# Kernel optimization log

Measured on AMD Instinct MI355X. Metric: run time of the kernel, lower is better.

The kernel has to match this reference:

```python
import jax, jax.numpy as jnp
import numpy as np

H, B, S, E, V, C = 1024, 1024, 128, 6, 3, 10


def setup_inputs() -> dict:
    key = jax.random.key(0)
    ks = jax.random.split(key, 18)
    sH = 1.0 / np.sqrt(H)

    def n(k, shape, scale):
        return (jax.random.normal(k, shape, dtype=jnp.float32) * scale)

    return {
        'x': jax.random.randint(ks[0], (B, S), 0, V),
        'emb': n(ks[1], (V, E), 1.0),
        'W_gx': n(ks[2], (H, E), 1.0 / np.sqrt(E)),
        'W_gh': n(ks[3], (H, H), sH),
        'b_g': n(ks[4], (H, 1), sH),
        'W_ix': n(ks[5], (H, E), 1.0 / np.sqrt(E)),
        'W_ih': n(ks[6], (H, H), sH),
        'b_i': n(ks[7], (H, 1), sH),
        'W_fx': n(ks[8], (H, E), 1.0 / np.sqrt(E)),
        'W_fh': n(ks[9], (H, H), sH),
        'b_f': n(ks[10], (H, 1), sH),
        'W_ox': n(ks[11], (H, E), 1.0 / np.sqrt(E)),
        'W_oh': n(ks[12], (H, H), sH),
        'b_o': n(ks[13], (H, 1), sH),
        'W_ph': n(ks[14], (C, H), sH),
        'b_p': n(ks[15], (C, 1), sH),
        'h_init': n(ks[16], (H, B), 1.0),
        'c_init': n(ks[17], (H, B), 1.0),
    }


def reference(x, emb, W_gx, W_gh, b_g, W_ix, W_ih, b_i, W_fx, W_fh, b_f,
              W_ox, W_oh, b_o, W_ph, b_p, h_init, c_init):
    T = x.shape[1] - 1  # torch loop runs over seq_length - 1 steps
    e = emb[x[:, :T]]  # [B, T, E]
    # Precompute all input-to-gate projections in one batched contraction each.
    Xg = jnp.einsum('he,bte->thb', W_gx, e)  # [T, H, B]
    Xi = jnp.einsum('he,bte->thb', W_ix, e)
    Xf = jnp.einsum('he,bte->thb', W_fx, e)
    Xo = jnp.einsum('he,bte->thb', W_ox, e)

    def step(carry, xs):
        h, c = carry  # [H, B]
        xg, xi, xf, xo = xs
        g = jnp.tanh(xg + W_gh @ h + b_g)
        i = jax.nn.sigmoid(xi + W_ih @ h + b_i)
        f = jax.nn.sigmoid(xf + W_fh @ h + b_f)
        o = jax.nn.sigmoid(xo + W_oh @ h + b_o)
        c2 = g * i + c * f
        h2 = jnp.tanh(c2) * o
        return (h2, c2), None

    (h, c), _ = jax.lax.scan(step, (h_init, c_init), (Xg, Xi, Xf, Xo))
    p = W_ph @ h + b_p  # [C, B]
    return jax.nn.log_softmax(p.T, axis=-1)  # [B, C]
```

## Files before the change

kernel.cpp:

```cpp
#include <hip/hip_runtime.h>

constexpr int kH = 1024;
constexpr int kB = 1024;
constexpr int kS = 128;
constexpr int kT = 127;
constexpr int kE = 6;
constexpr int kV = 3;
constexpr int kC = 10;

typedef short s16x8 __attribute__((ext_vector_type(8)));
typedef short s16x4 __attribute__((ext_vector_type(4)));
typedef float f32x4 __attribute__((ext_vector_type(4)));
typedef int   i32x2 __attribute__((ext_vector_type(2)));
typedef unsigned short u16;

__device__ __forceinline__ float b2f(u16 u) {
    return __uint_as_float(((unsigned)u) << 16);
}
__device__ __forceinline__ u16 f2b(float f) {
    unsigned u = __float_as_uint(f);
    return (u16)((u + 0x7FFFu + ((u >> 16) & 1u)) >> 16);
}
__device__ __forceinline__ float sigmoid_fast(float x) {
    return 1.0f / (1.0f + __expf(-x));
}
__device__ __forceinline__ float tanh_fast(float x) {
    return 2.0f / (1.0f + __expf(-2.0f * x)) - 1.0f;
}
__device__ __forceinline__ float clamp30(float x) {
    return fminf(fmaxf(x, -30.0f), 30.0f);
}

__device__ __forceinline__ void async_copy16(const u16* g, u16* l) {
    __builtin_amdgcn_global_load_lds(
        (const __attribute__((address_space(1))) void*)g,
        (__attribute__((address_space(3))) void*)l, 16, 0, 0);
}

__global__ __launch_bounds__(256) void prep_weights(
    const float* __restrict__ Wgh, const float* __restrict__ Wih,
    const float* __restrict__ Wfh, const float* __restrict__ Woh,
    u16* __restrict__ wsw)
{
    unsigned grp = blockIdx.x * 256 + threadIdx.x;
    const int lane = grp & 63;
    const int lm   = lane & 15;
    const int quad = lane >> 4;
    const int k0   = (grp >> 6) & 7;
    const int g    = (grp >> 9) & 3;
    const int kc   = (grp >> 11) & 3;
    const int by   = grp >> 13;
    const float* src = (g == 0) ? Wgh : (g == 1) ? Wih : (g == 2) ? Wfh : Woh;
    const int row = by * 16 + lm;
    const int k   = kc * 256 + k0 * 32 + quad * 8;
    f32x4 v0 = *(const f32x4*)(src + (size_t)row * kH + k);
    f32x4 v1 = *(const f32x4*)(src + (size_t)row * kH + k + 4);
    s16x8 o;
#pragma unroll
    for (int j = 0; j < 4; ++j) o[j] = (short)f2b(v0[j]);
#pragma unroll
    for (int j = 0; j < 4; ++j) o[4 + j] = (short)f2b(v1[j]);
    *(s16x8*)(wsw + (size_t)grp * 8) = o;
}

__global__ __launch_bounds__(1024) void prep_hc(
    const float* __restrict__ h0, const float* __restrict__ c0,
    u16* __restrict__ hA, float* __restrict__ cT)
{
    __shared__ float th[32][33];
    __shared__ float tc[32][33];
    int b = blockIdx.x * 32 + threadIdx.x;
    int h = blockIdx.y * 32 + threadIdx.y;
    th[threadIdx.y][threadIdx.x] = h0[(size_t)h * kB + b];
    tc[threadIdx.y][threadIdx.x] = c0[(size_t)h * kB + b];
    __syncthreads();
    int ob = blockIdx.x * 32 + threadIdx.y;
    int oh = blockIdx.y * 32 + threadIdx.x;
    hA[(size_t)ob * kH + oh] = f2b(th[threadIdx.x][threadIdx.y]);
    cT[(size_t)ob * kH + oh] = tc[threadIdx.x][threadIdx.y];
}

__global__ __launch_bounds__(256) void prep_q(
    const float* __restrict__ Wgx, const float* __restrict__ Wix,
    const float* __restrict__ Wfx, const float* __restrict__ Wox,
    const float* __restrict__ bg,  const float* __restrict__ bi,
    const float* __restrict__ bf_, const float* __restrict__ bo,
    const float* __restrict__ emb, float* __restrict__ Qp,
    int* __restrict__ ctrl)
{
    int tid = blockIdx.x * blockDim.x + threadIdx.x;
    if (tid < 512) ctrl[tid] = 0;
    if (tid >= 4096) return;
    int g   = tid >> 10;
    int hr4 = (tid & 1023) >> 2;
    int v   = tid & 3;
    const float* Wx = (g == 0) ? Wgx : (g == 1) ? Wix : (g == 2) ? Wfx : Wox;
    const float* bb = (g == 0) ? bg  : (g == 1) ? bi  : (g == 2) ? bf_ : bo;
    f32x4 o;
#pragma unroll
    for (int reg = 0; reg < 4; ++reg) {
        int row = hr4 * 4 + reg;
        float s = bb[row];
        if (v < kV) {
#pragma unroll
            for (int e = 0; e < kE; ++e) s += Wx[row * kE + e] * emb[v * kE + e];
        }
        o[reg] = s;
    }
    *(f32x4*)(Qp + (size_t)tid * 4) = o;
}

__global__ __launch_bounds__(512, 2) void lstm_persist(
    const u16* __restrict__ wsw, const float* __restrict__ Qp,
    const int* __restrict__ x,
    short* __restrict__ hA, short* __restrict__ hB,
    const float* __restrict__ cT, int* __restrict__ ctrl)
{
    __shared__ u16 wlds[65536];
    __shared__ int sh_ids[2];

    const int tid  = threadIdx.x;
    const int lane = tid & 63;
    const int wave = tid >> 6;
    const int lm   = lane & 15;
    const int quad = lane >> 4;

    if (tid == 0) {
        unsigned xccr;
        asm volatile("s_getreg_b32 %0, hwreg(HW_REG_XCC_ID)" : "=s"(xccr));
        int rank = atomicAdd(ctrl + 264 + (xccr & 7), 1);
        sh_ids[0] = (int)(xccr & 7);
        sh_ids[1] = rank;
    }
    __syncthreads();
    const int xcc  = sh_ids[0];
    const int rank = sh_ids[1];
    const int p    = xcc >> 1;
    const int q    = (xcc & 1) * 32 + rank;
    const bool leader = (rank == 0);
    const int r0 = q * 16;
    const int c0 = p * 256 + wave * 32;

    int* flags   = ctrl;
    int* release = ctrl + 256;

    const u16* wswblk = wsw + (size_t)q * 65536;

#pragma unroll
    for (int rr = 0; rr < 16; ++rr) {
        const int ub = wave * 8192 + rr * 512;
        async_copy16(wswblk + ub + lane * 8, &wlds[ub]);
    }

    f32x4 creg[2];
#pragma unroll
    for (int nt = 0; nt < 2; ++nt)
        creg[nt] = *(const f32x4*)(cT +
            (size_t)(c0 + nt * 16 + lm) * kH + r0 + quad * 4);

    const int* xp0 = x + (size_t)(c0 + lm) * kS;
    const int* xp1 = x + (size_t)(c0 + 16 + lm) * kS;
    const int koff = quad * 8;

    asm volatile("s_waitcnt vmcnt(0)" ::: "memory");
    __syncthreads();

#pragma unroll 1
    for (int t = 0; t < kT; ++t) {
        const short* hin  = (t & 1) ? hB : hA;
        short*       hout = (t & 1) ? hA : hB;

        const short* hrow0 = hin + (size_t)(c0 + lm) * kH + koff;
        const short* hrow1 = hin + (size_t)(c0 + 16 + lm) * kH + koff;
        s16x8 br[12][2];
#pragma unroll
        for (int s = 0; s < 10; ++s) {
            br[s][0] = *(const s16x8*)(hrow0 + s * 32);
            br[s][1] = *(const s16x8*)(hrow1 + s * 32);
        }

        int vv[2];
        {
            int v0 = xp0[t]; vv[0] = (v0 < 0) ? 0 : (v0 > kV - 1) ? (kV - 1) : v0;
            int v1 = xp1[t]; vv[1] = (v1 < 0) ? 0 : (v1 > kV - 1) ? (kV - 1) : v1;
        }
        f32x4 qv[2][4];
#pragma unroll
        for (int nt = 0; nt < 2; ++nt)
#pragma unroll
            for (int g = 0; g < 4; ++g)
                qv[nt][g] = *(const f32x4*)(Qp +
                    (size_t)(((g * 256 + q * 4 + quad) * 4 + vv[nt]) * 4));

        f32x4 acc[4][2];
        const f32x4 zero = {0.f, 0.f, 0.f, 0.f};
#pragma unroll
        for (int g = 0; g < 4; ++g)
#pragma unroll
            for (int n = 0; n < 2; ++n) acc[g][n] = zero;

#pragma unroll
        for (int k0 = 0; k0 < 32; ++k0) {
            if (k0 + 10 < 32) {
                const int s = (k0 + 10) % 12;
                br[s][0] = *(const s16x8*)(hrow0 + (k0 + 10) * 32);
                br[s][1] = *(const s16x8*)(hrow1 + (k0 + 10) * 32);
            }
            const int cur = k0 % 12;
            const int cb = (k0 >> 3) * 16384;
#pragma unroll
            for (int g = 0; g < 4; ++g) {
                const int f = cb + ((g * 8 + (k0 & 7)) * 64 + lane) * 8;
                s16x8 a = *(const s16x8*)&wlds[f];
                acc[g][0] = __builtin_amdgcn_mfma_f32_16x16x32_bf16(a, br[cur][0], acc[g][0], 0, 0, 0);
                acc[g][1] = __builtin_amdgcn_mfma_f32_16x16x32_bf16(a, br[cur][1], acc[g][1], 0, 0, 0);
            }
        }

#pragma unroll
        for (int nt = 0; nt < 2; ++nt) {
            const int c = c0 + nt * 16 + lm;
            const int rb = r0 + quad * 4;
            f32x4 cnew;
            s16x4 hnew;
#pragma unroll
            for (int reg = 0; reg < 4; ++reg) {
                float pg = clamp30(acc[0][nt][reg] + qv[nt][0][reg]);
                float pi = clamp30(acc[1][nt][reg] + qv[nt][1][reg]);
                float pf = clamp30(acc[2][nt][reg] + qv[nt][2][reg]);
                float po = clamp30(acc[3][nt][reg] + qv[nt][3][reg]);
                float gg = tanh_fast(pg);
                float ii = sigmoid_fast(pi);
                float ff = sigmoid_fast(pf);
                float oo = sigmoid_fast(po);
                float c2 = gg * ii + creg[nt][reg] * ff;
                c2 = fminf(fmaxf(c2, -200.0f), 200.0f);
                cnew[reg] = c2;
                hnew[reg] = (short)f2b(tanh_fast(c2) * oo);
            }
            creg[nt] = cnew;
            i32x2 hv;
            __builtin_memcpy(&hv, &hnew, 8);
            short* hp = hout + (size_t)c * kH + rb;
            asm volatile("global_store_dwordx2 %0, %1, off sc0 sc1"
                         :: "v"(hp), "v"(hv) : "memory");
        }

        if (t < kT - 1) {
            asm volatile("s_waitcnt vmcnt(0)" ::: "memory");
            __syncthreads();
            if (tid == 0) {
                int* fp = flags + p * 64 + q;
                int fv = t + 1;
                asm volatile("global_store_dword %0, %1, off sc0 sc1\n\t"
                             "s_waitcnt vmcnt(0)"
                             :: "v"(fp), "v"(fv) : "memory");
            }
            if (leader && tid < 64) {
                const int* fp = flags + p * 64 + lane;
                for (;;) {
                    int fvv;
                    asm volatile(
                        "global_load_dword %0, %1, off sc0 sc1\n\t"
                        "s_waitcnt vmcnt(0)"
                        : "=v"(fvv) : "v"(fp) : "memory");
                    if (__all(fvv > t)) break;
                    __builtin_amdgcn_s_sleep(1);
                }
                if (lane == 0) {
                    asm volatile("buffer_inv sc1\n\t"
                                 "s_waitcnt vmcnt(0)" ::: "memory");
                    int* rp = release + xcc;
                    int rv = t + 1;
                    asm volatile("global_store_dword %0, %1, off sc0 sc1\n\t"
                                 "s_waitcnt vmcnt(0)"
                                 :: "v"(rp), "v"(rv) : "memory");
                }
            }
            if (tid < 64) {
                const int* rp = release + xcc;
                for (;;) {
                    int rvv;
                    asm volatile(
                        "global_load_dword %0, %1, off sc0 sc1\n\t"
                        "s_waitcnt vmcnt(0)"
                        : "=v"(rvv) : "v"(rp) : "memory");
                    if (__all(rvv > t)) break;
                    __builtin_amdgcn_s_sleep(1);
                }
                asm volatile("buffer_inv" ::: "memory");
            }
            __syncthreads();
        }
    }
}

__global__ __launch_bounds__(256) void logits_kernel(
    const u16* __restrict__ hT, const float* __restrict__ Wph,
    const float* __restrict__ bp, float* __restrict__ out)
{
    const int wave = threadIdx.x >> 6;
    const int lane = threadIdx.x & 63;
    const int b = blockIdx.x * 4 + wave;

    const u16* hp = hT + (size_t)b * kH + lane * 16;
    float hf[16];
#pragma unroll
    for (int j = 0; j < 16; ++j) hf[j] = b2f(hp[j]);

    float p[kC];
#pragma unroll
    for (int cls = 0; cls < kC; ++cls) {
        const float* wp = Wph + (size_t)cls * kH + lane * 16;
        float s = 0.f;
#pragma unroll
        for (int j = 0; j < 16; ++j) s += hf[j] * wp[j];
#pragma unroll
        for (int off = 1; off < 64; off <<= 1) s += __shfl_xor(s, off, 64);
        p[cls] = fminf(fmaxf(s + bp[cls], -1.0e4f), 1.0e4f);
    }

    float m = p[0];
#pragma unroll
    for (int cls = 1; cls < kC; ++cls) m = fmaxf(m, p[cls]);
    float se = 0.f;
#pragma unroll
    for (int cls = 0; cls < kC; ++cls) se += __expf(p[cls] - m);
    float l = m + __logf(se);

    if (lane < kC) {
        float myp = p[0];
#pragma unroll
        for (int cls = 1; cls < kC; ++cls)
            if (lane == cls) myp = p[cls];
        out[(size_t)b * kC + lane] = myp - l;
    }
}

extern "C" void kernel_launch(void* const* d_in, const int* in_sizes, int n_in,
                              void* d_out, int out_size, void* d_ws, size_t ws_size,
                              hipStream_t stream)
{
    const int*   x   = (const int*)  d_in[0];
    const float* emb = (const float*)d_in[1];
    const float* Wgx = (const float*)d_in[2];
    const float* Wgh = (const float*)d_in[3];
    const float* bg  = (const float*)d_in[4];
    const float* Wix = (const float*)d_in[5];
    const float* Wih = (const float*)d_in[6];
    const float* bi  = (const float*)d_in[7];
    const float* Wfx = (const float*)d_in[8];
    const float* Wfh = (const float*)d_in[9];
    const float* bf_ = (const float*)d_in[10];
    const float* Wox = (const float*)d_in[11];
    const float* Woh = (const float*)d_in[12];
    const float* bo  = (const float*)d_in[13];
    const float* Wph = (const float*)d_in[14];
    const float* bp  = (const float*)d_in[15];
    const float* h0  = (const float*)d_in[16];
    const float* c0  = (const float*)d_in[17];

    char* ws = (char*)d_ws;
    float* Qp  = (float*)ws;
    u16*   hA  = (u16*)(ws + (64 << 10));
    u16*   hB  = hA + (size_t)kB * kH;
    float* cT  = (float*)(hB + (size_t)kB * kH);
    u16*   wsw = (u16*)(cT + (size_t)kB * kH);
    int*   ctrl = (int*)(wsw + (size_t)64 * 65536);

    prep_weights<<<dim3(2048), dim3(256), 0, stream>>>(Wgh, Wih, Wfh, Woh, wsw);
    prep_hc<<<dim3(kB / 32, kH / 32), dim3(32, 32), 0, stream>>>(h0, c0, hA, cT);
    prep_q<<<dim3(16), dim3(256), 0, stream>>>(Wgx, Wix, Wfx, Wox, bg, bi, bf_, bo,
                                               emb, Qp, ctrl);

    lstm_persist<<<dim3(256), dim3(512), 0, stream>>>(
        wsw, Qp, x, (short*)hA, (short*)hB, cT, ctrl);

    logits_kernel<<<dim3(kB / 4), dim3(256), 0, stream>>>(hB, Wph, bp, (float*)d_out);
}
```

Measured before the change: 2.523 ms.

## Use per-XCC local h buffers with pairwise partner flags and local counters

Each XCC now keeps its own copy of the hidden-state slab. Each block writes its slice of h into that XCC-local buffer with plain stores, and also writes it to the global h array. After a step, a block waits only on its partner block on the paired XCC, then copies the partner's h slice from global into the local buffer. A per-XCC counter replaces the leader/release barrier. The goal is to cut the cross-XCC all-to-all synchronisation and the uncached sc1 reads of h, and to read h from local L2. The cost is an extra copy step, a second block barrier and counter atomic per step, a smaller prefetch depth, and subtle memory-ordering assumptions about L2 coherence within an XCC.

```diff
diff --git a/kernel.cpp b/kernel.cpp
--- a/kernel.cpp
+++ b/kernel.cpp
@@ -12,6 +12,7 @@
 typedef short s16x4 __attribute__((ext_vector_type(4)));
 typedef float f32x4 __attribute__((ext_vector_type(4)));
 typedef int   i32x2 __attribute__((ext_vector_type(2)));
+typedef int   i32x4 __attribute__((ext_vector_type(4)));
 typedef unsigned short u16;
 
 __device__ __forceinline__ float b2f(u16 u) {
@@ -114,7 +115,8 @@
     const u16* __restrict__ wsw, const float* __restrict__ Qp,
     const int* __restrict__ x,
     short* __restrict__ hA, short* __restrict__ hB,
-    const float* __restrict__ cT, int* __restrict__ ctrl)
+    const float* __restrict__ cT, int* __restrict__ ctrl,
+    u16* __restrict__ xcb)
 {
     __shared__ u16 wlds[65536];
     __shared__ int sh_ids[2];
@@ -133,16 +135,18 @@
         sh_ids[1] = rank;
     }
     __syncthreads();
-    const int xcc  = sh_ids[0];
-    const int rank = sh_ids[1];
-    const int p    = xcc >> 1;
-    const int q    = (xcc & 1) * 32 + rank;
-    const bool leader = (rank == 0);
+    const int xcc   = sh_ids[0];
+    const int rank  = sh_ids[1];
+    const int p     = xcc >> 1;
+    const int side  = xcc & 1;
+    const int q     = side * 32 + rank;
+    const int qprt  = (1 - side) * 32 + rank;
     const int r0 = q * 16;
-    const int c0 = p * 256 + wave * 32;
-
-    int* flags   = ctrl;
-    int* release = ctrl + 256;
+    const int cl0 = wave * 32;
+    const int c0 = p * 256 + cl0;
+
+    int* pflag = ctrl;
+    int* lcnt  = ctrl + 256;
 
     const u16* wswblk = wsw + (size_t)q * 65536;
 
@@ -167,14 +171,40 @@
 
 #pragma unroll 1
     for (int t = 0; t < kT; ++t) {
-        const short* hin  = (t & 1) ? hB : hA;
-        short*       hout = (t & 1) ? hA : hB;
-
-        const short* hrow0 = hin + (size_t)(c0 + lm) * kH + koff;
-        const short* hrow1 = hin + (size_t)(c0 + 16 + lm) * kH + koff;
-        s16x8 br[12][2];
-#pragma unroll
-        for (int s = 0; s < 10; ++s) {
+        short* hout = (t & 1) ? hA : hB;
+        u16* xw = xcb + (size_t)(xcc * 2 + ((t + 1) & 1)) * 262144;
+
+        if (t >= 1) {
+            if (tid == 0) {
+                const int* cp = lcnt + xcc;
+                const int tgt = 64 * t;
+                for (;;) {
+                    int v;
+                    asm volatile("global_load_dword %0, %1, off sc0 sc1\n\t"
+                                 "s_waitcnt vmcnt(0)"
+                                 : "=v"(v) : "v"(cp) : "memory");
+                    if (v >= tgt) break;
+                    __builtin_amdgcn_s_sleep(1);
+                }
+            }
+            __syncthreads();
+            asm volatile("buffer_inv" ::: "memory");
+        }
+
+        const u16* xr = xcb + (size_t)(xcc * 2 + (t & 1)) * 262144;
+        const u16* hrow0;
+        const u16* hrow1;
+        if (t == 0) {
+            hrow0 = (const u16*)hA + (size_t)(c0 + lm) * kH + koff;
+            hrow1 = (const u16*)hA + (size_t)(c0 + 16 + lm) * kH + koff;
+        } else {
+            hrow0 = xr + (size_t)(cl0 + lm) * kH + koff;
+            hrow1 = xr + (size_t)(cl0 + 16 + lm) * kH + koff;
+        }
+
+        s16x8 br[8][2];
+#pragma unroll
+        for (int s = 0; s < 6; ++s) {
             br[s][0] = *(const s16x8*)(hrow0 + s * 32);
             br[s][1] = *(const s16x8*)(hrow1 + s * 32);
         }
@@ -201,12 +231,12 @@
 
 #pragma unroll
         for (int k0 = 0; k0 < 32; ++k0) {
-            if (k0 + 10 < 32) {
-                const int s = (k0 + 10) % 12;
-                br[s][0] = *(const s16x8*)(hrow0 + (k0 + 10) * 32);
-                br[s][1] = *(const s16x8*)(hrow1 + (k0 + 10) * 32);
-            }
-            const int cur = k0 % 12;
+            if (k0 + 6 < 32) {
+                const int s = (k0 + 6) & 7;
+                br[s][0] = *(const s16x8*)(hrow0 + (k0 + 6) * 32);
+                br[s][1] = *(const s16x8*)(hrow1 + (k0 + 6) * 32);
+            }
+            const int cur = k0 & 7;
             const int cb = (k0 >> 3) * 16384;
 #pragma unroll
             for (int g = 0; g < 4; ++g) {
@@ -219,7 +249,8 @@
 
 #pragma unroll
         for (int nt = 0; nt < 2; ++nt) {
-            const int c = c0 + nt * 16 + lm;
+            const int cl = cl0 + nt * 16 + lm;
+            const int c  = p * 256 + cl;
             const int rb = r0 + quad * 4;
             f32x4 cnew;
             s16x4 hnew;
@@ -244,53 +275,45 @@
             short* hp = hout + (size_t)c * kH + rb;
             asm volatile("global_store_dwordx2 %0, %1, off sc0 sc1"
                          :: "v"(hp), "v"(hv) : "memory");
+            *(s16x4*)(xw + (size_t)cl * kH + rb) = hnew;
         }
 
         if (t < kT - 1) {
             asm volatile("s_waitcnt vmcnt(0)" ::: "memory");
             __syncthreads();
             if (tid == 0) {
-                int* fp = flags + p * 64 + q;
+                int* fp = pflag + p * 64 + q;
                 int fv = t + 1;
                 asm volatile("global_store_dword %0, %1, off sc0 sc1\n\t"
                              "s_waitcnt vmcnt(0)"
                              :: "v"(fp), "v"(fv) : "memory");
-            }
-            if (leader && tid < 64) {
-                const int* fp = flags + p * 64 + lane;
+                atomicAdd(lcnt + xcc, 1);
+                const int* pp = pflag + p * 64 + qprt;
                 for (;;) {
-                    int fvv;
-                    asm volatile(
-                        "global_load_dword %0, %1, off sc0 sc1\n\t"
-                        "s_waitcnt vmcnt(0)"
-                        : "=v"(fvv) : "v"(fp) : "memory");
-                    if (__all(fvv > t)) break;
+                    int v;
+                    asm volatile("global_load_dword %0, %1, off sc0 sc1\n\t"
+                                 "s_waitcnt vmcnt(0)"
+                                 : "=v"(v) : "v"(pp) : "memory");
+                    if (v >= t + 1) break;
                     __builtin_amdgcn_s_sleep(1);
                 }
-                if (lane == 0) {
-                    asm volatile("buffer_inv sc1\n\t"
-                                 "s_waitcnt vmcnt(0)" ::: "memory");
-                    int* rp = release + xcc;
-                    int rv = t + 1;
-                    asm volatile("global_store_dword %0, %1, off sc0 sc1\n\t"
-                                 "s_waitcnt vmcnt(0)"
-                                 :: "v"(rp), "v"(rv) : "memory");
-                }
-            }
-            if (tid < 64) {
-                const int* rp = release + xcc;
-                for (;;) {
-                    int rvv;
-                    asm volatile(
-                        "global_load_dword %0, %1, off sc0 sc1\n\t"
-                        "s_waitcnt vmcnt(0)"
-                        : "=v"(rvv) : "v"(rp) : "memory");
-                    if (__all(rvv > t)) break;
-                    __builtin_amdgcn_s_sleep(1);
-                }
-                asm volatile("buffer_inv" ::: "memory");
             }
             __syncthreads();
+            {
+                const int cl   = tid >> 1;
+                const int half = tid & 1;
+                const short* src = hout + (size_t)(p * 256 + cl) * kH +
+                                   qprt * 16 + half * 8;
+                u16* dst = xw + (size_t)cl * kH + qprt * 16 + half * 8;
+                i32x4 v;
+                asm volatile("global_load_dwordx4 %0, %1, off sc0 sc1\n\t"
+                             "s_waitcnt vmcnt(0)"
+                             : "=v"(v) : "v"(src) : "memory");
+                *(i32x4*)dst = v;
+            }
+            asm volatile("s_waitcnt vmcnt(0)" ::: "memory");
+            __syncthreads();
+            if (tid == 0) atomicAdd(lcnt + xcc, 1);
         }
     }
 }
@@ -366,7 +389,8 @@
     u16*   hB  = hA + (size_t)kB * kH;
     float* cT  = (float*)(hB + (size_t)kB * kH);
     u16*   wsw = (u16*)(cT + (size_t)kB * kH);
-    int*   ctrl = (int*)(wsw + (size_t)64 * 65536);
+    u16*   xcb = wsw + (size_t)64 * 65536;
+    int*   ctrl = (int*)(xcb + (size_t)16 * 262144);
 
     prep_weights<<<dim3(2048), dim3(256), 0, stream>>>(Wgh, Wih, Wfh, Woh, wsw);
     prep_hc<<<dim3(kB / 32, kH / 32), dim3(32, 32), 0, stream>>>(h0, c0, hA, cT);
@@ -374,7 +398,7 @@
                                                emb, Qp, ctrl);
 
     lstm_persist<<<dim3(256), dim3(512), 0, stream>>>(
-        wsw, Qp, x, (short*)hA, (short*)hB, cT, ctrl);
+        wsw, Qp, x, (short*)hA, (short*)hB, cT, ctrl, xcb);
 
     logits_kernel<<<dim3(kB / 4), dim3(256), 0, stream>>>(hB, Wph, bp, (float*)d_out);
 }
```

Result: slower. 3.074 ms (+21.8%).
